# Kernel tuning notes

Hardware: AMD Instinct MI355X
Metric: run time of the kernel (lower is better)

The kernel has to match this reference:

```python
import jax, jax.numpy as jnp
import numpy as np

N_NODES = 100000


def setup_inputs() -> dict:
    key = jax.random.key(0)
    k1, k2, k3, k4 = jax.random.split(key, 4)
    E = 1600000
    in_dim, out_dim = 256, 64
    h = jax.random.normal(k1, (N_NODES, in_dim), dtype=jnp.float32)
    src = jax.random.randint(k2, (E,), 0, N_NODES, dtype=jnp.int64)
    dst = jax.random.randint(k3, (E,), 0, N_NODES, dtype=jnp.int64)
    W = jax.random.normal(k4, (in_dim, out_dim), dtype=jnp.float32) * (1.0 / np.sqrt(in_dim))
    b = jnp.zeros((out_dim,), dtype=jnp.float32)
    return {"h": h, "src": src, "dst": dst, "W": W, "b": b}


def reference(h, src, dst, W, b):
    # dgl GraphConv, norm='both': out = D_in^{-1/2} A D_out^{-1/2} h W + b
    E = src.shape[0]
    ones = jnp.ones((E,), dtype=h.dtype)
    deg_out = jax.ops.segment_sum(ones, src, num_segments=N_NODES)  # out-degree of src nodes
    deg_in = jax.ops.segment_sum(ones, dst, num_segments=N_NODES)   # in-degree of dst nodes
    norm_src = jnp.clip(deg_out, 1.0, None) ** -0.5                  # [N]
    norm_dst = jnp.clip(deg_in, 1.0, None) ** -0.5                   # [N]
    # in_dim > out_dim: project first (as dgl does), then aggregate small features
    x = (h * norm_src[:, None]) @ W                                  # [N, out_dim]
    msgs = x[src]                                                    # [E, out_dim] gather
    agg = jax.ops.segment_sum(msgs, dst, num_segments=N_NODES)      # [N, out_dim] scatter-add
    out = agg * norm_dst[:, None] + b
    # ReLU; dropout is identity in eval mode
    return jax.nn.relu(out)
```

## Files before the change

kernel.cpp:

```cpp
#include <hip/hip_runtime.h>
#include <hip/hip_fp16.h>

#define N_NODES 100000
#define IN_DIM 256
#define OUT_DIM 64
#define NT 782
#define NSC 512
#define SMAX 3200
#define CAP_F 3072
#define GEMM_BLKS 1563

typedef _Float16 half8 __attribute__((ext_vector_type(8)));
typedef float f32x4 __attribute__((ext_vector_type(4)));

__global__ __launch_bounds__(256) void init_kernel(int* __restrict__ cursorD,
                                                   int* __restrict__ cursorS) {
    int i = blockIdx.x * 256 + threadIdx.x;
    if (i < NT) { cursorD[i] = 0; cursorS[i] = 0; }
}

#define A_LD 136
__global__ __launch_bounds__(256) void fused_kernel(const int* __restrict__ src,
                                                    const int* __restrict__ dst,
                                                    int* __restrict__ cursorD,
                                                    int* __restrict__ cursorS,
                                                    int* __restrict__ binnedD,
                                                    unsigned char* __restrict__ srcb,
                                                    const float* __restrict__ hmat,
                                                    const float* __restrict__ W,
                                                    __half* __restrict__ xh,
                                                    int E, int chunk) {
    __shared__ char smem[47568];
    const int t = threadIdx.x;
    if (blockIdx.x < NSC) {
        int* sorted            = (int*)(smem);
        int* histD             = (int*)(smem + 12800);
        int* boffD             = (int*)(smem + 15928);
        int* resvD             = (int*)(smem + 19056);
        int* histS             = (int*)(smem + 22184);
        int* boffS             = (int*)(smem + 25312);
        int* resvS             = (int*)(smem + 28440);
        unsigned short* sbin   = (unsigned short*)(smem + 31568);
        unsigned short* sbinS  = (unsigned short*)(smem + 37968);
        unsigned char* sortedB = (unsigned char*)(smem + 44368);
        const int blk = blockIdx.x;
        const int lane = t & 63, wv = t >> 6;
        const int lo = blk * chunk;
        int hiA = lo + chunk; if (hiA > E) hiA = E;
        for (int s0 = lo; s0 < hiA; s0 += SMAX) {
            int m = hiA - s0; if (m > SMAX) m = SMAX;
            for (int i = t; i < NT; i += 256) { histD[i] = 0; histS[i] = 0; }
            __syncthreads();
            for (int k = t; k < m; k += 256) {
                int s = src[s0 + k], d = dst[s0 + k];
                atomicAdd(&histD[d >> 7], 1);
                atomicAdd(&histS[s >> 7], 1);
            }
            __syncthreads();
            if (wv < 2) {
                int* hsrc = (wv == 0) ? histD : histS;
                int* bdst = (wv == 0) ? boffD : boffS;
                int carry = 0;
                for (int r = 0; r < (NT + 63) / 64; ++r) {
                    int i = r * 64 + lane;
                    int v = (i < NT) ? hsrc[i] : 0;
                    int incl = v;
#pragma unroll
                    for (int off = 1; off < 64; off <<= 1) {
                        int y = __shfl_up(incl, off);
                        if (lane >= off) incl += y;
                    }
                    if (i < NT) bdst[i] = carry + incl - v;
                    carry += __shfl(incl, 63);
                }
            }
            __syncthreads();
            for (int i = t; i < NT; i += 256) {
                int hd = histD[i];
                if (hd) resvD[i] = atomicAdd(&cursorD[i], hd);
                int hs = histS[i];
                if (hs) resvS[i] = atomicAdd(&cursorS[i], hs);
                histD[i] = boffD[i];
                histS[i] = boffS[i];
            }
            __syncthreads();
            for (int k = t; k < m; k += 256) {
                int s = src[s0 + k], d = dst[s0 + k];
                int bd = d >> 7;
                int p = atomicAdd(&histD[bd], 1);
                sorted[p] = (s << 7) | (d & 127);
                sbin[p] = (unsigned short)bd;
                int bs = s >> 7;
                int ps = atomicAdd(&histS[bs], 1);
                sortedB[ps] = (unsigned char)(s & 127);
                sbinS[ps] = (unsigned short)bs;
            }
            __syncthreads();
            for (int k = t; k < m; k += 256) {
                int b = sbin[k];
                int loc = resvD[b] + (k - boffD[b]);
                if (loc < CAP_F) binnedD[b * CAP_F + loc] = sorted[k];
                int bs = sbinS[k];
                int locS = resvS[bs] + (k - boffS[bs]);
                if (locS < CAP_F) srcb[bs * CAP_F + locS] = sortedB[k];
            }
            __syncthreads();
        }
    } else {
        _Float16* sA = (_Float16*)(smem);
        _Float16* sB = (_Float16*)(smem + 64 * A_LD * 2);
        const int lane = t & 63;
        const int w = t >> 6;
        const int row0 = (blockIdx.x - NSC) * 64;
        const int m0 = (w & 1) * 32;
        const int n0 = (w >> 1) * 32;

        f32x4 acc00 = {0.f, 0.f, 0.f, 0.f}, acc01 = {0.f, 0.f, 0.f, 0.f};
        f32x4 acc10 = {0.f, 0.f, 0.f, 0.f}, acc11 = {0.f, 0.f, 0.f, 0.f};

        for (int khalf = 0; khalf < 2; ++khalf) {
            const int k0 = khalf * 128;
            __syncthreads();
#pragma unroll
            for (int it = 0; it < 8; ++it) {
                int f = t + it * 256;
                int row = f >> 5;
                int c4 = f & 31;
                int grow = row0 + row; if (grow >= N_NODES) grow = N_NODES - 1;
                float4 v = *(const float4*)(hmat + (size_t)grow * IN_DIM + k0 + c4 * 4);
                _Float16 p[4];
                p[0] = (_Float16)v.x; p[1] = (_Float16)v.y;
                p[2] = (_Float16)v.z; p[3] = (_Float16)v.w;
                *(uint2*)&sA[row * A_LD + c4 * 4] = *(uint2*)p;
            }
            {
                int n = t & 63;
                int kk0 = (t >> 6) * 32;
#pragma unroll
                for (int kb = 0; kb < 8; ++kb) {
                    _Float16 p[4];
#pragma unroll
                    for (int u = 0; u < 4; ++u)
                        p[u] = (_Float16)W[(size_t)(k0 + kk0 + kb * 4 + u) * OUT_DIM + n];
                    *(uint2*)&sB[n * A_LD + kk0 + kb * 4] = *(uint2*)p;
                }
            }
            __syncthreads();
#pragma unroll
            for (int kb = 0; kb < 4; ++kb) {
                int koff = kb * 32 + (lane >> 4) * 8;
                half8 a0 = *(const half8*)&sA[(m0 + (lane & 15)) * A_LD + koff];
                half8 a1 = *(const half8*)&sA[(m0 + 16 + (lane & 15)) * A_LD + koff];
                half8 b0 = *(const half8*)&sB[(n0 + (lane & 15)) * A_LD + koff];
                half8 b1 = *(const half8*)&sB[(n0 + 16 + (lane & 15)) * A_LD + koff];
                acc00 = __builtin_amdgcn_mfma_f32_16x16x32_f16(a0, b0, acc00, 0, 0, 0);
                acc01 = __builtin_amdgcn_mfma_f32_16x16x32_f16(a0, b1, acc01, 0, 0, 0);
                acc10 = __builtin_amdgcn_mfma_f32_16x16x32_f16(a1, b0, acc10, 0, 0, 0);
                acc11 = __builtin_amdgcn_mfma_f32_16x16x32_f16(a1, b1, acc11, 0, 0, 0);
            }
        }

        const int col16 = lane & 15;
        const int rq = (lane >> 4) * 4;
#pragma unroll
        for (int mi = 0; mi < 2; ++mi) {
#pragma unroll
            for (int ni = 0; ni < 2; ++ni) {
                const f32x4 a = (mi == 0) ? (ni == 0 ? acc00 : acc01)
                                          : (ni == 0 ? acc10 : acc11);
                int col = n0 + ni * 16 + col16;
#pragma unroll
                for (int r = 0; r < 4; ++r) {
                    int row = row0 + m0 + mi * 16 + rq + r;
                    if (row < N_NODES)
                        xh[(size_t)row * OUT_DIM + col] = __float2half(a[r]);
                }
            }
        }
    }
}

__global__ __launch_bounds__(256) void tile_kernel(const int* __restrict__ cursorD,
                                                   const int* __restrict__ cursorS,
                                                   const int* __restrict__ binnedD,
                                                   const unsigned char* __restrict__ srcb,
                                                   int* __restrict__ csr,
                                                   int* __restrict__ offs, int* __restrict__ cnt,
                                                   float* __restrict__ nrmS) {
    __shared__ int h[128], cur[128];
    __shared__ int lcsr[CAP_F];
    __shared__ int w0tot;
    const int bin = blockIdx.x, t = threadIdx.x, lane = t & 63;
    if (t < 128) h[t] = 0;
    __syncthreads();

    const int base = bin * CAP_F;
    int m = cursorD[bin]; if (m > CAP_F) m = CAP_F;
    for (int k = t; k < m; k += 256) atomicAdd(&h[binnedD[base + k] & 127], 1);
    __syncthreads();
    int v = (t < 128) ? h[t] : 0;
    int incl = v;
#pragma unroll
    for (int off = 1; off < 64; off <<= 1) {
        int y = __shfl_up(incl, off);
        if (lane >= off) incl += y;
    }
    if (t == 63) w0tot = incl;
    __syncthreads();
    int excl = incl - v + ((t >= 64 && t < 128) ? w0tot : 0);
    if (t < 128) {
        cur[t] = excl;
        int node = bin * 128 + t;
        if (node < N_NODES) { offs[node] = base + excl; cnt[node] = v; }
    }
    __syncthreads();
    for (int k = t; k < m; k += 256) {
        int rec = binnedD[base + k];
        int p = atomicAdd(&cur[rec & 127], 1);
        lcsr[p] = rec >> 7;
    }
    __syncthreads();
    for (int k = t; k < m; k += 256) csr[base + k] = lcsr[k];

    __syncthreads();
    if (t < 128) h[t] = 0;
    __syncthreads();
    int ms = cursorS[bin]; if (ms > CAP_F) ms = CAP_F;
    const int sbase = bin * CAP_F;
    for (int k = t; k < ms; k += 256) atomicAdd(&h[srcb[sbase + k]], 1);
    __syncthreads();
    if (t < 128) {
        int node = bin * 128 + t;
        if (node < N_NODES) {
            int d = h[t];
            nrmS[node] = rsqrtf((float)(d < 1 ? 1 : d));
        }
    }
}

__global__ __launch_bounds__(256) void aggregate_kernel(const int* __restrict__ offs,
                                                        const int* __restrict__ cnt,
                                                        const int* __restrict__ csr,
                                                        const float* __restrict__ nrmS,
                                                        const __half* __restrict__ xh,
                                                        const float* __restrict__ b,
                                                        float* __restrict__ out) {
    const int t = threadIdx.x;
    const int lane = t & 63;
    const int wid = t >> 6;
    const int node = blockIdx.x * 4 + wid;
    const int g = lane >> 3;
    const int c = lane & 7;

    const int start = offs[node];
    const int n = cnt[node];

    float acc[8] = {0.f, 0.f, 0.f, 0.f, 0.f, 0.f, 0.f, 0.f};
    for (int base = 0; base < n; base += 64) {
        int k = base + lane;
        int sidx = (k < n) ? csr[start + k] : 0;
        int m = n - base; if (m > 64) m = 64;
        for (int e0 = 0; e0 < m; e0 += 16) {
            int ea = e0 + g;
            int eb = e0 + 8 + g;
            int sa = __shfl(sidx, ea);
            int sb = __shfl(sidx, eb);
            bool va = ea < m;
            bool vb = eb < m;
            float wa = va ? nrmS[sa] : 0.f;
            uint4 ra = *(const uint4*)(xh + (size_t)(va ? sa : 0) * OUT_DIM + 8 * c);
            const bool grpb = (e0 + 8) < m;
            uint4 rb;
            float wb = 0.f;
            if (grpb) {
                wb = vb ? nrmS[sb] : 0.f;
                rb = *(const uint4*)(xh + (size_t)(vb ? sb : 0) * OUT_DIM + 8 * c);
            }
            {
                const __half2* hp = (const __half2*)&ra;
#pragma unroll
                for (int p = 0; p < 4; ++p) {
                    float2 f = __half22float2(hp[p]);
                    acc[2 * p]     = fmaf(wa, f.x, acc[2 * p]);
                    acc[2 * p + 1] = fmaf(wa, f.y, acc[2 * p + 1]);
                }
            }
            if (grpb) {
                const __half2* hp = (const __half2*)&rb;
#pragma unroll
                for (int p = 0; p < 4; ++p) {
                    float2 f = __half22float2(hp[p]);
                    acc[2 * p]     = fmaf(wb, f.x, acc[2 * p]);
                    acc[2 * p + 1] = fmaf(wb, f.y, acc[2 * p + 1]);
                }
            }
        }
    }

#pragma unroll
    for (int off = 8; off < 64; off <<= 1) {
#pragma unroll
        for (int p = 0; p < 8; ++p)
            acc[p] += __shfl_xor(acc[p], off);
    }

    if (g == 0) {
        float nrm = rsqrtf((float)(n < 1 ? 1 : n));
        float4 bv0 = *(const float4*)&b[c * 8];
        float4 bv1 = *(const float4*)&b[c * 8 + 4];
        float4 r0, r1;
        r0.x = fmaxf(fmaf(acc[0], nrm, bv0.x), 0.f);
        r0.y = fmaxf(fmaf(acc[1], nrm, bv0.y), 0.f);
        r0.z = fmaxf(fmaf(acc[2], nrm, bv0.z), 0.f);
        r0.w = fmaxf(fmaf(acc[3], nrm, bv0.w), 0.f);
        r1.x = fmaxf(fmaf(acc[4], nrm, bv1.x), 0.f);
        r1.y = fmaxf(fmaf(acc[5], nrm, bv1.y), 0.f);
        r1.z = fmaxf(fmaf(acc[6], nrm, bv1.z), 0.f);
        r1.w = fmaxf(fmaf(acc[7], nrm, bv1.w), 0.f);
        float4* orow = (float4*)(out + (size_t)node * OUT_DIM + c * 8);
        orow[0] = r0;
        orow[1] = r1;
    }
}

extern "C" void kernel_launch(void* const* d_in, const int* in_sizes, int n_in,
                              void* d_out, int out_size, void* d_ws, size_t ws_size,
                              hipStream_t stream) {
    const float* h   = (const float*)d_in[0];
    const int*   src = (const int*)d_in[1];
    const int*   dst = (const int*)d_in[2];
    const float* W   = (const float*)d_in[3];
    const float* b   = (const float*)d_in[4];
    float* out = (float*)d_out;
    const int E = in_sizes[1];
    const int chunkS = (E + NSC - 1) / NSC;

    char* ws = (char*)d_ws;
    int*           cursorD = (int*)(ws);
    int*           cursorS = (int*)(ws + 3328);
    int*           binnedD = (int*)(ws + 6656);
    int*           csr     = binnedD;
    unsigned char* srcb    = (unsigned char*)(ws + 9615872);
    int*           offs    = (int*)(ws + 12018176);
    int*           cntA    = (int*)(ws + 12418176);
    float*         nrmS    = (float*)(ws + 12818176);
    __half*        xh      = (__half*)(ws + 13218176);

    init_kernel<<<4, 256, 0, stream>>>(cursorD, cursorS);
    fused_kernel<<<NSC + GEMM_BLKS, 256, 0, stream>>>(src, dst, cursorD, cursorS,
                                                      binnedD, srcb, h, W, xh, E, chunkS);
    tile_kernel<<<NT, 256, 0, stream>>>(cursorD, cursorS, binnedD, srcb, csr, offs, cntA, nrmS);
    aggregate_kernel<<<N_NODES / 4, 256, 0, stream>>>(offs, cntA, csr, nrmS, xh, b, out);
}
```

Baseline: 253.6 us.

## Replace local sort-then-scatter binning with direct atomic-reserved scatter

The edge-binning blocks no longer sort each chunk locally in shared memory before writing to global bins. Instead they build a per-bin histogram, reserve global ranges with one atomic per bin, then scatter each edge directly using shared-memory atomics for its slot. This drops the prefix scan, the staging arrays and several barriers, and shrinks shared memory to the GEMM's needs, which may raise occupancy. The cost is uncoalesced scattered global writes where the old version wrote contiguous runs, and src/dst are read twice per block.

```diff
diff --git a/kernel.cpp b/kernel.cpp
--- a/kernel.cpp
+++ b/kernel.cpp
@@ -6,9 +6,10 @@
 #define OUT_DIM 64
 #define NT 782
 #define NSC 512
-#define SMAX 3200
 #define CAP_F 3072
 #define GEMM_BLKS 1563
+#define A_LD 136
+#define FUSED_LDS (64 * A_LD * 2 * 2)
 
 typedef _Float16 half8 __attribute__((ext_vector_type(8)));
 typedef float f32x4 __attribute__((ext_vector_type(4)));
@@ -19,7 +20,6 @@
     if (i < NT) { cursorD[i] = 0; cursorS[i] = 0; }
 }
 
-#define A_LD 136
 __global__ __launch_bounds__(256) void fused_kernel(const int* __restrict__ src,
                                                     const int* __restrict__ dst,
                                                     int* __restrict__ cursorD,
@@ -30,81 +30,36 @@
                                                     const float* __restrict__ W,
                                                     __half* __restrict__ xh,
                                                     int E, int chunk) {
-    __shared__ char smem[47568];
+    __shared__ char smem[FUSED_LDS];
     const int t = threadIdx.x;
     if (blockIdx.x < NSC) {
-        int* sorted            = (int*)(smem);
-        int* histD             = (int*)(smem + 12800);
-        int* boffD             = (int*)(smem + 15928);
-        int* resvD             = (int*)(smem + 19056);
-        int* histS             = (int*)(smem + 22184);
-        int* boffS             = (int*)(smem + 25312);
-        int* resvS             = (int*)(smem + 28440);
-        unsigned short* sbin   = (unsigned short*)(smem + 31568);
-        unsigned short* sbinS  = (unsigned short*)(smem + 37968);
-        unsigned char* sortedB = (unsigned char*)(smem + 44368);
+        int* histD = (int*)(smem);
+        int* histS = (int*)(smem + 3136);
         const int blk = blockIdx.x;
-        const int lane = t & 63, wv = t >> 6;
         const int lo = blk * chunk;
-        int hiA = lo + chunk; if (hiA > E) hiA = E;
-        for (int s0 = lo; s0 < hiA; s0 += SMAX) {
-            int m = hiA - s0; if (m > SMAX) m = SMAX;
-            for (int i = t; i < NT; i += 256) { histD[i] = 0; histS[i] = 0; }
-            __syncthreads();
-            for (int k = t; k < m; k += 256) {
-                int s = src[s0 + k], d = dst[s0 + k];
-                atomicAdd(&histD[d >> 7], 1);
-                atomicAdd(&histS[s >> 7], 1);
-            }
-            __syncthreads();
-            if (wv < 2) {
-                int* hsrc = (wv == 0) ? histD : histS;
-                int* bdst = (wv == 0) ? boffD : boffS;
-                int carry = 0;
-                for (int r = 0; r < (NT + 63) / 64; ++r) {
-                    int i = r * 64 + lane;
-                    int v = (i < NT) ? hsrc[i] : 0;
-                    int incl = v;
-#pragma unroll
-                    for (int off = 1; off < 64; off <<= 1) {
-                        int y = __shfl_up(incl, off);
-                        if (lane >= off) incl += y;
-                    }
-                    if (i < NT) bdst[i] = carry + incl - v;
-                    carry += __shfl(incl, 63);
-                }
-            }
-            __syncthreads();
-            for (int i = t; i < NT; i += 256) {
-                int hd = histD[i];
-                if (hd) resvD[i] = atomicAdd(&cursorD[i], hd);
-                int hs = histS[i];
-                if (hs) resvS[i] = atomicAdd(&cursorS[i], hs);
-                histD[i] = boffD[i];
-                histS[i] = boffS[i];
-            }
-            __syncthreads();
-            for (int k = t; k < m; k += 256) {
-                int s = src[s0 + k], d = dst[s0 + k];
-                int bd = d >> 7;
-                int p = atomicAdd(&histD[bd], 1);
-                sorted[p] = (s << 7) | (d & 127);
-                sbin[p] = (unsigned short)bd;
-                int bs = s >> 7;
-                int ps = atomicAdd(&histS[bs], 1);
-                sortedB[ps] = (unsigned char)(s & 127);
-                sbinS[ps] = (unsigned short)bs;
-            }
-            __syncthreads();
-            for (int k = t; k < m; k += 256) {
-                int b = sbin[k];
-                int loc = resvD[b] + (k - boffD[b]);
-                if (loc < CAP_F) binnedD[b * CAP_F + loc] = sorted[k];
-                int bs = sbinS[k];
-                int locS = resvS[bs] + (k - boffS[bs]);
-                if (locS < CAP_F) srcb[bs * CAP_F + locS] = sortedB[k];
-            }
-            __syncthreads();
+        int hi = lo + chunk; if (hi > E) hi = E;
+        for (int i = t; i < NT; i += 256) { histD[i] = 0; histS[i] = 0; }
+        __syncthreads();
+        for (int k = lo + t; k < hi; k += 256) {
+            atomicAdd(&histD[dst[k] >> 7], 1);
+            atomicAdd(&histS[src[k] >> 7], 1);
+        }
+        __syncthreads();
+        for (int i = t; i < NT; i += 256) {
+            int hd = histD[i];
+            histD[i] = hd ? atomicAdd(&cursorD[i], hd) : 0;
+            int hs = histS[i];
+            histS[i] = hs ? atomicAdd(&cursorS[i], hs) : 0;
+        }
+        __syncthreads();
+        for (int k = lo + t; k < hi; k += 256) {
+            int s = src[k], d = dst[k];
+            int bd = d >> 7;
+            int p = atomicAdd(&histD[bd], 1);
+            if (p < CAP_F) binnedD[bd * CAP_F + p] = (s << 7) | (d & 127);
+            int bs = s >> 7;
+            int ps = atomicAdd(&histS[bs], 1);
+            if (ps < CAP_F) srcb[bs * CAP_F + ps] = (unsigned char)(s & 127);
         }
     } else {
         _Float16* sA = (_Float16*)(smem);
```

Result: slower. 262.9 us (+3.7%).

## Fuse CSR tiling into aggregation and compute out-degree with global atomics

Applied to the files above, without the earlier changes.

Out-degree is no longer found by binning source indices in LDS and histogramming per bin. It is now counted directly with global atomics into a deg_out array, and the source-norm is computed on the fly from it during aggregation. The tile and aggregate kernels are merged: each block rebuilds the local CSR for half of a 128-node dst bin in LDS and aggregates directly, with no global csr, offs or cnt round-trip and one fewer launch. The costs are 1.6M global atomics scattered over 100K counters and each bin's CSR being rebuilt twice, once per split. Aggregation also drops from one wave per node across 25K blocks to 16 nodes per wave across 1564 blocks, which may hurt latency hiding.

```diff
diff --git a/kernel.cpp b/kernel.cpp
--- a/kernel.cpp
+++ b/kernel.cpp
@@ -9,68 +9,62 @@
 #define SMAX 3200
 #define CAP_F 3072
 #define GEMM_BLKS 1563
+#define NSPLIT 2
+#define A_LD 136
+#define FUSED_LDS (64 * A_LD * 2 * 2)
 
 typedef _Float16 half8 __attribute__((ext_vector_type(8)));
 typedef float f32x4 __attribute__((ext_vector_type(4)));
 
 __global__ __launch_bounds__(256) void init_kernel(int* __restrict__ cursorD,
-                                                   int* __restrict__ cursorS) {
+                                                   int* __restrict__ deg_out) {
     int i = blockIdx.x * 256 + threadIdx.x;
-    if (i < NT) { cursorD[i] = 0; cursorS[i] = 0; }
+    if (i < N_NODES) deg_out[i] = 0;
+    if (i < NT) cursorD[i] = 0;
 }
 
-#define A_LD 136
 __global__ __launch_bounds__(256) void fused_kernel(const int* __restrict__ src,
                                                     const int* __restrict__ dst,
                                                     int* __restrict__ cursorD,
-                                                    int* __restrict__ cursorS,
                                                     int* __restrict__ binnedD,
-                                                    unsigned char* __restrict__ srcb,
+                                                    int* __restrict__ deg_out,
                                                     const float* __restrict__ hmat,
                                                     const float* __restrict__ W,
                                                     __half* __restrict__ xh,
                                                     int E, int chunk) {
-    __shared__ char smem[47568];
+    __shared__ char smem[FUSED_LDS];
     const int t = threadIdx.x;
     if (blockIdx.x < NSC) {
-        int* sorted            = (int*)(smem);
-        int* histD             = (int*)(smem + 12800);
-        int* boffD             = (int*)(smem + 15928);
-        int* resvD             = (int*)(smem + 19056);
-        int* histS             = (int*)(smem + 22184);
-        int* boffS             = (int*)(smem + 25312);
-        int* resvS             = (int*)(smem + 28440);
-        unsigned short* sbin   = (unsigned short*)(smem + 31568);
-        unsigned short* sbinS  = (unsigned short*)(smem + 37968);
-        unsigned char* sortedB = (unsigned char*)(smem + 44368);
+        int* sorted          = (int*)(smem);
+        unsigned short* sbin = (unsigned short*)(smem + 12800);
+        int* histD           = (int*)(smem + 19200);
+        int* boffD           = (int*)(smem + 22328);
+        int* resvD           = (int*)(smem + 25456);
         const int blk = blockIdx.x;
         const int lane = t & 63, wv = t >> 6;
         const int lo = blk * chunk;
         int hiA = lo + chunk; if (hiA > E) hiA = E;
         for (int s0 = lo; s0 < hiA; s0 += SMAX) {
             int m = hiA - s0; if (m > SMAX) m = SMAX;
-            for (int i = t; i < NT; i += 256) { histD[i] = 0; histS[i] = 0; }
+            for (int i = t; i < NT; i += 256) histD[i] = 0;
             __syncthreads();
             for (int k = t; k < m; k += 256) {
-                int s = src[s0 + k], d = dst[s0 + k];
-                atomicAdd(&histD[d >> 7], 1);
-                atomicAdd(&histS[s >> 7], 1);
-            }
-            __syncthreads();
-            if (wv < 2) {
-                int* hsrc = (wv == 0) ? histD : histS;
-                int* bdst = (wv == 0) ? boffD : boffS;
+                atomicAdd(&deg_out[src[s0 + k]], 1);
+                atomicAdd(&histD[dst[s0 + k] >> 7], 1);
+            }
+            __syncthreads();
+            if (wv == 0) {
                 int carry = 0;
                 for (int r = 0; r < (NT + 63) / 64; ++r) {
                     int i = r * 64 + lane;
-                    int v = (i < NT) ? hsrc[i] : 0;
+                    int v = (i < NT) ? histD[i] : 0;
                     int incl = v;
 #pragma unroll
                     for (int off = 1; off < 64; off <<= 1) {
                         int y = __shfl_up(incl, off);
                         if (lane >= off) incl += y;
                     }
-                    if (i < NT) bdst[i] = carry + incl - v;
+                    if (i < NT) boffD[i] = carry + incl - v;
                     carry += __shfl(incl, 63);
                 }
             }
@@ -78,10 +72,7 @@
             for (int i = t; i < NT; i += 256) {
                 int hd = histD[i];
                 if (hd) resvD[i] = atomicAdd(&cursorD[i], hd);
-                int hs = histS[i];
-                if (hs) resvS[i] = atomicAdd(&cursorS[i], hs);
                 histD[i] = boffD[i];
-                histS[i] = boffS[i];
             }
             __syncthreads();
             for (int k = t; k < m; k += 256) {
@@ -90,19 +81,12 @@
                 int p = atomicAdd(&histD[bd], 1);
                 sorted[p] = (s << 7) | (d & 127);
                 sbin[p] = (unsigned short)bd;
-                int bs = s >> 7;
-                int ps = atomicAdd(&histS[bs], 1);
-                sortedB[ps] = (unsigned char)(s & 127);
-                sbinS[ps] = (unsigned short)bs;
             }
             __syncthreads();
             for (int k = t; k < m; k += 256) {
                 int b = sbin[k];
                 int loc = resvD[b] + (k - boffD[b]);
                 if (loc < CAP_F) binnedD[b * CAP_F + loc] = sorted[k];
-                int bs = sbinS[k];
-                int locS = resvS[bs] + (k - boffS[bs]);
-                if (locS < CAP_F) srcb[bs * CAP_F + locS] = sortedB[k];
             }
             __syncthreads();
         }
@@ -180,20 +164,21 @@
     }
 }
 
-__global__ __launch_bounds__(256) void tile_kernel(const int* __restrict__ cursorD,
-                                                   const int* __restrict__ cursorS,
-                                                   const int* __restrict__ binnedD,
-                                                   const unsigned char* __restrict__ srcb,
-                                                   int* __restrict__ csr,
-                                                   int* __restrict__ offs, int* __restrict__ cnt,
-                                                   float* __restrict__ nrmS) {
-    __shared__ int h[128], cur[128];
+__global__ __launch_bounds__(256) void agg_kernel(const int* __restrict__ cursorD,
+                                                  const int* __restrict__ binnedD,
+                                                  const int* __restrict__ deg_out,
+                                                  const __half* __restrict__ xh,
+                                                  const float* __restrict__ b,
+                                                  float* __restrict__ out) {
     __shared__ int lcsr[CAP_F];
+    __shared__ int h[128], cur[128], loff[128], lcnt[128];
     __shared__ int w0tot;
-    const int bin = blockIdx.x, t = threadIdx.x, lane = t & 63;
+    const int bin = blockIdx.x / NSPLIT;
+    const int half = blockIdx.x % NSPLIT;
+    const int t = threadIdx.x, lane = t & 63, wv = t >> 6;
+
     if (t < 128) h[t] = 0;
     __syncthreads();
-
     const int base = bin * CAP_F;
     int m = cursorD[bin]; if (m > CAP_F) m = CAP_F;
     for (int k = t; k < m; k += 256) atomicAdd(&h[binnedD[base + k] & 127], 1);
@@ -208,11 +193,7 @@
     if (t == 63) w0tot = incl;
     __syncthreads();
     int excl = incl - v + ((t >= 64 && t < 128) ? w0tot : 0);
-    if (t < 128) {
-        cur[t] = excl;
-        int node = bin * 128 + t;
-        if (node < N_NODES) { offs[node] = base + excl; cnt[node] = v; }
-    }
+    if (t < 128) { loff[t] = excl; lcnt[t] = v; cur[t] = excl; }
     __syncthreads();
     for (int k = t; k < m; k += 256) {
         int rec = binnedD[base + k];
@@ -220,106 +201,86 @@
         lcsr[p] = rec >> 7;
     }
     __syncthreads();
-    for (int k = t; k < m; k += 256) csr[base + k] = lcsr[k];
-
-    __syncthreads();
-    if (t < 128) h[t] = 0;
-    __syncthreads();
-    int ms = cursorS[bin]; if (ms > CAP_F) ms = CAP_F;
-    const int sbase = bin * CAP_F;
-    for (int k = t; k < ms; k += 256) atomicAdd(&h[srcb[sbase + k]], 1);
-    __syncthreads();
-    if (t < 128) {
-        int node = bin * 128 + t;
-        if (node < N_NODES) {
-            int d = h[t];
-            nrmS[node] = rsqrtf((float)(d < 1 ? 1 : d));
-        }
-    }
-}
-
-__global__ __launch_bounds__(256) void aggregate_kernel(const int* __restrict__ offs,
-                                                        const int* __restrict__ cnt,
-                                                        const int* __restrict__ csr,
-                                                        const float* __restrict__ nrmS,
-                                                        const __half* __restrict__ xh,
-                                                        const float* __restrict__ b,
-                                                        float* __restrict__ out) {
-    const int t = threadIdx.x;
-    const int lane = t & 63;
-    const int wid = t >> 6;
-    const int node = blockIdx.x * 4 + wid;
+
     const int g = lane >> 3;
     const int c = lane & 7;
-
-    const int start = offs[node];
-    const int n = cnt[node];
-
-    float acc[8] = {0.f, 0.f, 0.f, 0.f, 0.f, 0.f, 0.f, 0.f};
-    for (int base = 0; base < n; base += 64) {
-        int k = base + lane;
-        int sidx = (k < n) ? csr[start + k] : 0;
-        int m = n - base; if (m > 64) m = 64;
-        for (int e0 = 0; e0 < m; e0 += 16) {
-            int ea = e0 + g;
-            int eb = e0 + 8 + g;
-            int sa = __shfl(sidx, ea);
-            int sb = __shfl(sidx, eb);
-            bool va = ea < m;
-            bool vb = eb < m;
-            float wa = va ? nrmS[sa] : 0.f;
-            uint4 ra = *(const uint4*)(xh + (size_t)(va ? sa : 0) * OUT_DIM + 8 * c);
-            const bool grpb = (e0 + 8) < m;
-            uint4 rb;
-            float wb = 0.f;
-            if (grpb) {
-                wb = vb ? nrmS[sb] : 0.f;
-                rb = *(const uint4*)(xh + (size_t)(vb ? sb : 0) * OUT_DIM + 8 * c);
-            }
-            {
-                const __half2* hp = (const __half2*)&ra;
-#pragma unroll
-                for (int p = 0; p < 4; ++p) {
-                    float2 f = __half22float2(hp[p]);
-                    acc[2 * p]     = fmaf(wa, f.x, acc[2 * p]);
-                    acc[2 * p + 1] = fmaf(wa, f.y, acc[2 * p + 1]);
-                }
-            }
-            if (grpb) {
-                const __half2* hp = (const __half2*)&rb;
-#pragma unroll
-                for (int p = 0; p < 4; ++p) {
-                    float2 f = __half22float2(hp[p]);
-                    acc[2 * p]     = fmaf(wb, f.x, acc[2 * p]);
-                    acc[2 * p + 1] = fmaf(wb, f.y, acc[2 * p + 1]);
-                }
-            }
-        }
-    }
-
-#pragma unroll
-    for (int off = 8; off < 64; off <<= 1) {
-#pragma unroll
-        for (int p = 0; p < 8; ++p)
-            acc[p] += __shfl_xor(acc[p], off);
-    }
-
-    if (g == 0) {
-        float nrm = rsqrtf((float)(n < 1 ? 1 : n));
-        float4 bv0 = *(const float4*)&b[c * 8];
-        float4 bv1 = *(const float4*)&b[c * 8 + 4];
-        float4 r0, r1;
-        r0.x = fmaxf(fmaf(acc[0], nrm, bv0.x), 0.f);
-        r0.y = fmaxf(fmaf(acc[1], nrm, bv0.y), 0.f);
-        r0.z = fmaxf(fmaf(acc[2], nrm, bv0.z), 0.f);
-        r0.w = fmaxf(fmaf(acc[3], nrm, bv0.w), 0.f);
-        r1.x = fmaxf(fmaf(acc[4], nrm, bv1.x), 0.f);
-        r1.y = fmaxf(fmaf(acc[5], nrm, bv1.y), 0.f);
-        r1.z = fmaxf(fmaf(acc[6], nrm, bv1.z), 0.f);
-        r1.w = fmaxf(fmaf(acc[7], nrm, bv1.w), 0.f);
-        float4* orow = (float4*)(out + (size_t)node * OUT_DIM + c * 8);
-        orow[0] = r0;
-        orow[1] = r1;
+    for (int idx = 0; idx < 16; ++idx) {
+        const int nloc = half * 64 + wv * 16 + idx;
+        const int node = bin * 128 + nloc;
+        if (node >= N_NODES) continue;
+        const int start = loff[nloc];
+        const int n = lcnt[nloc];
+
+        float acc[8] = {0.f, 0.f, 0.f, 0.f, 0.f, 0.f, 0.f, 0.f};
+        for (int bb = 0; bb < n; bb += 64) {
+            int k = bb + lane;
+            int sidx = (k < n) ? lcsr[start + k] : 0;
+            int mm = n - bb; if (mm > 64) mm = 64;
+            for (int e0 = 0; e0 < mm; e0 += 16) {
+                int ea = e0 + g;
+                int eb = e0 + 8 + g;
+                int sa = __shfl(sidx, ea);
+                int sb = __shfl(sidx, eb);
+                bool va = ea < mm;
+                bool vb = eb < mm;
+                int sa0 = va ? sa : 0;
+                int dga = deg_out[sa0];
+                float wa = va ? rsqrtf((float)(dga < 1 ? 1 : dga)) : 0.f;
+                uint4 ra = *(const uint4*)(xh + (size_t)sa0 * OUT_DIM + 8 * c);
+                const bool grpb = (e0 + 8) < mm;
+                uint4 rb;
+                float wb = 0.f;
+                if (grpb) {
+                    int sb0 = vb ? sb : 0;
+                    int dgb = deg_out[sb0];
+                    wb = vb ? rsqrtf((float)(dgb < 1 ? 1 : dgb)) : 0.f;
+                    rb = *(const uint4*)(xh + (size_t)sb0 * OUT_DIM + 8 * c);
+                }
+                {
+                    const __half2* hp = (const __half2*)&ra;
+#pragma unroll
+                    for (int p = 0; p < 4; ++p) {
+                        float2 f = __half22float2(hp[p]);
+                        acc[2 * p]     = fmaf(wa, f.x, acc[2 * p]);
+                        acc[2 * p + 1] = fmaf(wa, f.y, acc[2 * p + 1]);
+                    }
+                }
+                if (grpb) {
+                    const __half2* hp = (const __half2*)&rb;
+#pragma unroll
+                    for (int p = 0; p < 4; ++p) {
+                        float2 f = __half22float2(hp[p]);
+                        acc[2 * p]     = fmaf(wb, f.x, acc[2 * p]);
+                        acc[2 * p + 1] = fmaf(wb, f.y, acc[2 * p + 1]);
+                    }
+                }
+            }
+        }
+
+#pragma unroll
+        for (int off = 8; off < 64; off <<= 1) {
+#pragma unroll
+            for (int p = 0; p < 8; ++p)
+                acc[p] += __shfl_xor(acc[p], off);
+        }
+
+        if (g == 0) {
+            float nrm = rsqrtf((float)(n < 1 ? 1 : n));
+            float4 bv0 = *(const float4*)&b[c * 8];
+            float4 bv1 = *(const float4*)&b[c * 8 + 4];
+            float4 r0, r1;
+            r0.x = fmaxf(fmaf(acc[0], nrm, bv0.x), 0.f);
+            r0.y = fmaxf(fmaf(acc[1], nrm, bv0.y), 0.f);
+            r0.z = fmaxf(fmaf(acc[2], nrm, bv0.z), 0.f);
+            r0.w = fmaxf(fmaf(acc[3], nrm, bv0.w), 0.f);
+            r1.x = fmaxf(fmaf(acc[4], nrm, bv1.x), 0.f);
+            r1.y = fmaxf(fmaf(acc[5], nrm, bv1.y), 0.f);
+            r1.z = fmaxf(fmaf(acc[6], nrm, bv1.z), 0.f);
+            r1.w = fmaxf(fmaf(acc[7], nrm, bv1.w), 0.f);
+            float4* orow = (float4*)(out + (size_t)node * OUT_DIM + c * 8);
+            orow[0] = r0;
+            orow[1] = r1;
+        }
     }
 }
 
@@ -336,19 +297,13 @@
     const int chunkS = (E + NSC - 1) / NSC;
 
     char* ws = (char*)d_ws;
-    int*           cursorD = (int*)(ws);
-    int*           cursorS = (int*)(ws + 3328);
-    int*           binnedD = (int*)(ws + 6656);
-    int*           csr     = binnedD;
-    unsigned char* srcb    = (unsigned char*)(ws + 9615872);
-    int*           offs    = (int*)(ws + 12018176);
-    int*           cntA    = (int*)(ws + 12418176);
-    float*         nrmS    = (float*)(ws + 12818176);
-    __half*        xh      = (__half*)(ws + 13218176);
-
-    init_kernel<<<4, 256, 0, stream>>>(cursorD, cursorS);
-    fused_kernel<<<NSC + GEMM_BLKS, 256, 0, stream>>>(src, dst, cursorD, cursorS,
-                                                      binnedD, srcb, h, W, xh, E, chunkS);
-    tile_kernel<<<NT, 256, 0, stream>>>(cursorD, cursorS, binnedD, srcb, csr, offs, cntA, nrmS);
-    aggregate_kernel<<<N_NODES / 4, 256, 0, stream>>>(offs, cntA, csr, nrmS, xh, b, out);
+    int*    cursorD = (int*)(ws);
+    int*    deg_out = (int*)(ws + 3328);
+    int*    binnedD = (int*)(ws + 403328);
+    __half* xh      = (__half*)(ws + 10012544);
+
+    init_kernel<<<(N_NODES + 255) / 256, 256, 0, stream>>>(cursorD, deg_out);
+    fused_kernel<<<NSC + GEMM_BLKS, 256, 0, stream>>>(src, dst, cursorD, binnedD, deg_out,
+                                                      h, W, xh, E, chunkS);
+    agg_kernel<<<NT * NSPLIT, 256, 0, stream>>>(cursorD, binnedD, deg_out, xh, b, out);
 }
```

Result: slower. 284.1 us (+12.0%).

## Fuse CSR tile build into aggregation and pre-scale xh by source norm

Applied to the files above, without the earlier changes.

The tile kernel is split. A new scale kernel computes source-degree norms per bin and multiplies them into the half-precision projected features in place. The aggregation kernel now builds each bin's CSR in LDS and aggregates straight from it, which drops the global csr/offs/cnt/nrmS writes and the per-edge nrmS gathers. The cost is that each of the NSPLIT blocks per bin repeats the histogram and local sort, and the in-place rescale adds an extra read-write pass over xh plus one more fp16 rounding.

```diff
diff --git a/kernel.cpp b/kernel.cpp
--- a/kernel.cpp
+++ b/kernel.cpp
@@ -9,6 +9,9 @@
 #define SMAX 3200
 #define CAP_F 3072
 #define GEMM_BLKS 1563
+#define NSPLIT 4
+#define A_LD 136
+#define FUSED_LDS 47568
 
 typedef _Float16 half8 __attribute__((ext_vector_type(8)));
 typedef float f32x4 __attribute__((ext_vector_type(4)));
@@ -19,7 +22,6 @@
     if (i < NT) { cursorD[i] = 0; cursorS[i] = 0; }
 }
 
-#define A_LD 136
 __global__ __launch_bounds__(256) void fused_kernel(const int* __restrict__ src,
                                                     const int* __restrict__ dst,
                                                     int* __restrict__ cursorD,
@@ -30,7 +32,7 @@
                                                     const float* __restrict__ W,
                                                     __half* __restrict__ xh,
                                                     int E, int chunk) {
-    __shared__ char smem[47568];
+    __shared__ char smem[FUSED_LDS];
     const int t = threadIdx.x;
     if (blockIdx.x < NSC) {
         int* sorted            = (int*)(smem);
@@ -180,20 +182,54 @@
     }
 }
 
-__global__ __launch_bounds__(256) void tile_kernel(const int* __restrict__ cursorD,
-                                                   const int* __restrict__ cursorS,
-                                                   const int* __restrict__ binnedD,
-                                                   const unsigned char* __restrict__ srcb,
-                                                   int* __restrict__ csr,
-                                                   int* __restrict__ offs, int* __restrict__ cnt,
-                                                   float* __restrict__ nrmS) {
-    __shared__ int h[128], cur[128];
+__global__ __launch_bounds__(256) void scale_kernel(const int* __restrict__ cursorS,
+                                                    const unsigned char* __restrict__ srcb,
+                                                    __half* __restrict__ xh) {
+    __shared__ int h[128];
+    __shared__ float sc[128];
+    const int bin = blockIdx.x, t = threadIdx.x;
+    if (t < 128) h[t] = 0;
+    __syncthreads();
+    int ms = cursorS[bin]; if (ms > CAP_F) ms = CAP_F;
+    const int sbase = bin * CAP_F;
+    for (int k = t; k < ms; k += 256) atomicAdd(&h[srcb[sbase + k]], 1);
+    __syncthreads();
+    if (t < 128) {
+        int d = h[t];
+        sc[t] = rsqrtf((float)(d < 1 ? 1 : d));
+    }
+    __syncthreads();
+    const int node0 = bin * 128;
+    for (int i = t; i < 128 * 16; i += 256) {
+        int r = i >> 4, q = i & 15;
+        int node = node0 + r;
+        if (node < N_NODES) {
+            __half2* p = (__half2*)(xh + (size_t)node * OUT_DIM + q * 4);
+            float s = sc[r];
+            __half2 a0 = p[0], a1 = p[1];
+            float2 f0 = __half22float2(a0), f1 = __half22float2(a1);
+            __half2 r0, r1;
+            r0.x = __float2half(f0.x * s); r0.y = __float2half(f0.y * s);
+            r1.x = __float2half(f1.x * s); r1.y = __float2half(f1.y * s);
+            p[0] = r0; p[1] = r1;
+        }
+    }
+}
+
+__global__ __launch_bounds__(256) void agg_kernel(const int* __restrict__ cursorD,
+                                                  const int* __restrict__ binnedD,
+                                                  const __half* __restrict__ xh,
+                                                  const float* __restrict__ b,
+                                                  float* __restrict__ out) {
     __shared__ int lcsr[CAP_F];
+    __shared__ int h[128], cur[128], loff[128], lcnt[128];
     __shared__ int w0tot;
-    const int bin = blockIdx.x, t = threadIdx.x, lane = t & 63;
+    const int bin = blockIdx.x / NSPLIT;
+    const int part = blockIdx.x % NSPLIT;
+    const int t = threadIdx.x, lane = t & 63, wv = t >> 6;
+
     if (t < 128) h[t] = 0;
     __syncthreads();
-
     const int base = bin * CAP_F;
     int m = cursorD[bin]; if (m > CAP_F) m = CAP_F;
     for (int k = t; k < m; k += 256) atomicAdd(&h[binnedD[base + k] & 127], 1);
@@ -208,11 +244,7 @@
     if (t == 63) w0tot = incl;
     __syncthreads();
     int excl = incl - v + ((t >= 64 && t < 128) ? w0tot : 0);
-    if (t < 128) {
-        cur[t] = excl;
-        int node = bin * 128 + t;
-        if (node < N_NODES) { offs[node] = base + excl; cnt[node] = v; }
-    }
+    if (t < 128) { loff[t] = excl; lcnt[t] = v; cur[t] = excl; }
     __syncthreads();
     for (int k = t; k < m; k += 256) {
         int rec = binnedD[base + k];
@@ -220,61 +252,32 @@
         lcsr[p] = rec >> 7;
     }
     __syncthreads();
-    for (int k = t; k < m; k += 256) csr[base + k] = lcsr[k];
-
-    __syncthreads();
-    if (t < 128) h[t] = 0;
-    __syncthreads();
-    int ms = cursorS[bin]; if (ms > CAP_F) ms = CAP_F;
-    const int sbase = bin * CAP_F;
-    for (int k = t; k < ms; k += 256) atomicAdd(&h[srcb[sbase + k]], 1);
-    __syncthreads();
-    if (t < 128) {
-        int node = bin * 128 + t;
-        if (node < N_NODES) {
-            int d = h[t];
-            nrmS[node] = rsqrtf((float)(d < 1 ? 1 : d));
-        }
-    }
-}
-
-__global__ __launch_bounds__(256) void aggregate_kernel(const int* __restrict__ offs,
-                                                        const int* __restrict__ cnt,
-                                                        const int* __restrict__ csr,
-                                                        const float* __restrict__ nrmS,
-                                                        const __half* __restrict__ xh,
-                                                        const float* __restrict__ b,
-                                                        float* __restrict__ out) {
-    const int t = threadIdx.x;
-    const int lane = t & 63;
-    const int wid = t >> 6;
-    const int node = blockIdx.x * 4 + wid;
+
     const int g = lane >> 3;
     const int c = lane & 7;
-
-    const int start = offs[node];
-    const int n = cnt[node];
-
-    float acc[8] = {0.f, 0.f, 0.f, 0.f, 0.f, 0.f, 0.f, 0.f};
-    for (int base = 0; base < n; base += 64) {
-        int k = base + lane;
-        int sidx = (k < n) ? csr[start + k] : 0;
-        int m = n - base; if (m > 64) m = 64;
-        for (int e0 = 0; e0 < m; e0 += 16) {
+    for (int idx = 0; idx < 8; ++idx) {
+        const int nloc = part * 32 + wv * 8 + idx;
+        const int node = bin * 128 + nloc;
+        if (node >= N_NODES) continue;
+        const int start = loff[nloc];
+        const int n = lcnt[nloc];
+
+        float acc[8] = {0.f, 0.f, 0.f, 0.f, 0.f, 0.f, 0.f, 0.f};
+        for (int e0 = 0; e0 < n; e0 += 16) {
             int ea = e0 + g;
-            int eb = e0 + 8 + g;
-            int sa = __shfl(sidx, ea);
-            int sb = __shfl(sidx, eb);
-            bool va = ea < m;
-            bool vb = eb < m;
-            float wa = va ? nrmS[sa] : 0.f;
-            uint4 ra = *(const uint4*)(xh + (size_t)(va ? sa : 0) * OUT_DIM + 8 * c);
-            const bool grpb = (e0 + 8) < m;
+            int eb = ea + 8;
+            bool va = ea < n;
+            bool vb = eb < n;
+            int sa0 = va ? lcsr[start + ea] : 0;
+            float wa = va ? 1.f : 0.f;
+            uint4 ra = *(const uint4*)(xh + (size_t)sa0 * OUT_DIM + 8 * c);
+            const bool grpb = (e0 + 8) < n;
             uint4 rb;
             float wb = 0.f;
             if (grpb) {
-                wb = vb ? nrmS[sb] : 0.f;
-                rb = *(const uint4*)(xh + (size_t)(vb ? sb : 0) * OUT_DIM + 8 * c);
+                int sb0 = vb ? lcsr[start + eb] : 0;
+                wb = vb ? 1.f : 0.f;
+                rb = *(const uint4*)(xh + (size_t)sb0 * OUT_DIM + 8 * c);
             }
             {
                 const __half2* hp = (const __half2*)&ra;
@@ -295,31 +298,31 @@
                 }
             }
         }
-    }
-
-#pragma unroll
-    for (int off = 8; off < 64; off <<= 1) {
-#pragma unroll
-        for (int p = 0; p < 8; ++p)
-            acc[p] += __shfl_xor(acc[p], off);
-    }
-
-    if (g == 0) {
-        float nrm = rsqrtf((float)(n < 1 ? 1 : n));
-        float4 bv0 = *(const float4*)&b[c * 8];
-        float4 bv1 = *(const float4*)&b[c * 8 + 4];
-        float4 r0, r1;
-        r0.x = fmaxf(fmaf(acc[0], nrm, bv0.x), 0.f);
-        r0.y = fmaxf(fmaf(acc[1], nrm, bv0.y), 0.f);
-        r0.z = fmaxf(fmaf(acc[2], nrm, bv0.z), 0.f);
-        r0.w = fmaxf(fmaf(acc[3], nrm, bv0.w), 0.f);
-        r1.x = fmaxf(fmaf(acc[4], nrm, bv1.x), 0.f);
-        r1.y = fmaxf(fmaf(acc[5], nrm, bv1.y), 0.f);
-        r1.z = fmaxf(fmaf(acc[6], nrm, bv1.z), 0.f);
-        r1.w = fmaxf(fmaf(acc[7], nrm, bv1.w), 0.f);
-        float4* orow = (float4*)(out + (size_t)node * OUT_DIM + c * 8);
-        orow[0] = r0;
-        orow[1] = r1;
+
+#pragma unroll
+        for (int off = 8; off < 64; off <<= 1) {
+#pragma unroll
+            for (int p = 0; p < 8; ++p)
+                acc[p] += __shfl_xor(acc[p], off);
+        }
+
+        if (g == 0) {
+            float nrm = rsqrtf((float)(n < 1 ? 1 : n));
+            float4 bv0 = *(const float4*)&b[c * 8];
+            float4 bv1 = *(const float4*)&b[c * 8 + 4];
+            float4 r0, r1;
+            r0.x = fmaxf(fmaf(acc[0], nrm, bv0.x), 0.f);
+            r0.y = fmaxf(fmaf(acc[1], nrm, bv0.y), 0.f);
+            r0.z = fmaxf(fmaf(acc[2], nrm, bv0.z), 0.f);
+            r0.w = fmaxf(fmaf(acc[3], nrm, bv0.w), 0.f);
+            r1.x = fmaxf(fmaf(acc[4], nrm, bv1.x), 0.f);
+            r1.y = fmaxf(fmaf(acc[5], nrm, bv1.y), 0.f);
+            r1.z = fmaxf(fmaf(acc[6], nrm, bv1.z), 0.f);
+            r1.w = fmaxf(fmaf(acc[7], nrm, bv1.w), 0.f);
+            float4* orow = (float4*)(out + (size_t)node * OUT_DIM + c * 8);
+            orow[0] = r0;
+            orow[1] = r1;
+        }
     }
 }
 
@@ -339,16 +342,12 @@
     int*           cursorD = (int*)(ws);
     int*           cursorS = (int*)(ws + 3328);
     int*           binnedD = (int*)(ws + 6656);
-    int*           csr     = binnedD;
     unsigned char* srcb    = (unsigned char*)(ws + 9615872);
-    int*           offs    = (int*)(ws + 12018176);
-    int*           cntA    = (int*)(ws + 12418176);
-    float*         nrmS    = (float*)(ws + 12818176);
-    __half*        xh      = (__half*)(ws + 13218176);
+    __half*        xh      = (__half*)(ws + 12018176);
 
     init_kernel<<<4, 256, 0, stream>>>(cursorD, cursorS);
     fused_kernel<<<NSC + GEMM_BLKS, 256, 0, stream>>>(src, dst, cursorD, cursorS,
                                                       binnedD, srcb, h, W, xh, E, chunkS);
-    tile_kernel<<<NT, 256, 0, stream>>>(cursorD, cursorS, binnedD, srcb, csr, offs, cntA, nrmS);
-    aggregate_kernel<<<N_NODES / 4, 256, 0, stream>>>(offs, cntA, csr, nrmS, xh, b, out);
-}
+    scale_kernel<<<NT, 256, 0, stream>>>(cursorS, srcb, xh);
+    agg_kernel<<<NT * NSPLIT, 256, 0, stream>>>(cursorD, binnedD, xh, b, out);
+}
```

Result: no change. 252.5 us (-0.4%).
